# Kernel optimization log

Hardware: AMD Instinct MI355X
Metric: run time of the kernel (lower is better)

Reference implementation:

```python
import jax, jax.numpy as jnp
import numpy as np


def setup_inputs() -> dict:
    key = jax.random.key(0)
    k1, k2 = jax.random.split(key)
    B, T, C = 32, 1024, 384
    MAX_LEN = 8192
    x = jax.random.normal(k1, (B, T, C), dtype=jnp.float32)
    duration = jax.random.randint(k2, (B, T), 0, 8, dtype=jnp.int64)
    return {"x": x, "duration": duration, "max_len": MAX_LEN}


def reference(x, duration, max_len):
    # x: [B, T, C] float; duration: [B, T] int frame counts; max_len: python int.
    # Equivalent of per-row repeat_interleave(x, duration) followed by zero-pad
    # to max_len, done as one fused cumsum + searchsorted + gather.
    B, T, C = x.shape
    cum = jnp.cumsum(duration, axis=1)            # [B, T] end frame of each phoneme
    mel_len = cum[:, -1]                          # [B] total expanded length
    pos = jnp.arange(max_len)                     # [max_len] output frame indices
    # For output frame j, source phoneme = first i with cum[i] > j
    idx = jax.vmap(lambda c: jnp.searchsorted(c, pos, side="right"))(cum)  # [B, max_len]
    idx = jnp.minimum(idx, T - 1)
    mask = pos[None, :] < mel_len[:, None]        # [B, max_len] valid (non-pad) frames
    out = jnp.take_along_axis(x, idx[:, :, None], axis=1)  # [B, max_len, C]
    out = jnp.where(mask[:, :, None], out, jnp.zeros((), dtype=x.dtype))
    return out, mel_len
```

## Files before the change

### kernel.cpp

```cpp
#include <hip/hip_runtime.h>


#define BB 32
#define TT 1024
#define CC 384
#define MAXLEN 8192
#define OUT0 (BB * MAXLEN * CC)

typedef float f32x4 __attribute__((ext_vector_type(4)));

__global__ void lr_prep(const int* __restrict__ dur,
                        int* __restrict__ idx,
                        float* __restrict__ mel_out) {
    __shared__ int lds[TT];
    const int b = blockIdx.x;
    const int t = threadIdx.x;
    lds[t] = dur[b * TT + t];
    __syncthreads();
    for (int off = 1; off < TT; off <<= 1) {
        int v = (t >= off) ? lds[t - off] : 0;
        __syncthreads();
        lds[t] += v;
        __syncthreads();
    }
    const int ml = lds[TT - 1];
    if (t == TT - 1) mel_out[b] = (float)ml;

    #pragma unroll
    for (int k = 0; k < MAXLEN / TT; ++k) {
        int p = t + k * TT;
        int r = -1;
        if (p < ml) {
            int lo = 0, hi = TT;
            while (lo < hi) {
                int mid = (lo + hi) >> 1;
                if (lds[mid] <= p) lo = mid + 1; else hi = mid;
            }
            r = (lo < TT - 1) ? lo : (TT - 1);
        }
        idx[b * MAXLEN + p] = r;
    }
}

__global__ void lr_gather(const f32x4* __restrict__ x4,
                          const int* __restrict__ idx,
                          f32x4* __restrict__ out4) {
    const unsigned QPR = CC / 4;
    const unsigned HALF = (unsigned)BB * MAXLEN * QPR / 2;
    const unsigned stride = gridDim.x * blockDim.x;
    for (unsigned q = blockIdx.x * blockDim.x + threadIdx.x; q < HALF; q += stride) {
        const unsigned q2 = q + HALF;
        unsigned row1 = q / QPR,  lane1 = q  - row1 * QPR;
        unsigned row2 = q2 / QPR, lane2 = q2 - row2 * QPR;
        int i1 = idx[row1];
        int i2 = idx[row2];
        f32x4 v1 = (f32x4)0.f, v2 = (f32x4)0.f;
        if (i1 >= 0) v1 = x4[((row1 >> 13) * TT + (unsigned)i1) * QPR + lane1];
        if (i2 >= 0) v2 = x4[((row2 >> 13) * TT + (unsigned)i2) * QPR + lane2];
        __builtin_nontemporal_store(v1, &out4[q]);
        __builtin_nontemporal_store(v2, &out4[q2]);
    }
}

extern "C" void kernel_launch(void* const* d_in, const int* in_sizes, int n_in,
                              void* d_out, int out_size, void* d_ws, size_t ws_size,
                              hipStream_t stream) {
    const float* x   = (const float*)d_in[0];
    const int*   dur = (const int*)d_in[1];
    float* out = (float*)d_out;

    int* idx = (int*)d_ws;

    lr_prep<<<BB, TT, 0, stream>>>(dur, idx, out + OUT0);
    lr_gather<<<4096, 256, 0, stream>>>((const f32x4*)x, idx, (f32x4*)out);
}
```

Before: 86.11 us.

## Fuse duration scan and gather into one per-chunk kernel

Replaces the separate prep kernel and the global idx buffer with a single kernel. Each block handles one batch row's 256-frame chunk, recomputes the duration prefix sum in LDS, binary-searches its chunk's source indices into shared memory, then streams the gather. This removes a kernel launch, the serialization between the two kernels, and the idx round trip through global memory. The cost is redundant scan work in every block, and the grid shape changes from grid-stride to fixed per-chunk tiling.

```diff
diff --git a/kernel.cpp b/kernel.cpp
--- a/kernel.cpp
+++ b/kernel.cpp
@@ -6,59 +6,73 @@
 #define CC 384
 #define MAXLEN 8192
 #define OUT0 (BB * MAXLEN * CC)
+#define NT 512
+#define ROWS_PER_BLK 256
+#define NCHUNK (MAXLEN / ROWS_PER_BLK)
+#define QPR (CC / 4)
+#define QPB (ROWS_PER_BLK * QPR)
+#define ITERS (QPB / NT)
 
 typedef float f32x4 __attribute__((ext_vector_type(4)));
 
-__global__ void lr_prep(const int* __restrict__ dur,
-                        int* __restrict__ idx,
-                        float* __restrict__ mel_out) {
-    __shared__ int lds[TT];
-    const int b = blockIdx.x;
-    const int t = threadIdx.x;
-    lds[t] = dur[b * TT + t];
+__global__ __launch_bounds__(NT) void lr_fused(const int* __restrict__ dur,
+                                               const f32x4* __restrict__ x4,
+                                               f32x4* __restrict__ out4,
+                                               float* __restrict__ mel_out) {
+    __shared__ int sd[TT];
+    __shared__ int ss[NT];
+    __shared__ int sidx[ROWS_PER_BLK];
+    const int b     = blockIdx.y;
+    const int chunk = blockIdx.x;
+    const int t     = threadIdx.x;
+
+    sd[t]      = dur[b * TT + t];
+    sd[t + NT] = dur[b * TT + t + NT];
     __syncthreads();
-    for (int off = 1; off < TT; off <<= 1) {
-        int v = (t >= off) ? lds[t - off] : 0;
+    ss[t] = sd[2 * t] + sd[2 * t + 1];
+    __syncthreads();
+    #pragma unroll
+    for (int off = 1; off < NT; off <<= 1) {
+        int v = (t >= off) ? ss[t - off] : 0;
         __syncthreads();
-        lds[t] += v;
+        ss[t] += v;
         __syncthreads();
     }
-    const int ml = lds[TT - 1];
-    if (t == TT - 1) mel_out[b] = (float)ml;
+    int inc = ss[t];
+    int d1  = sd[2 * t + 1];
+    __syncthreads();
+    sd[2 * t + 1] = inc;
+    sd[2 * t]     = inc - d1;
+    __syncthreads();
+    const int ml = sd[TT - 1];
+    if (chunk == 0 && t == 0) mel_out[b] = (float)ml;
 
-    #pragma unroll
-    for (int k = 0; k < MAXLEN / TT; ++k) {
-        int p = t + k * TT;
+    if (t < ROWS_PER_BLK) {
+        int p = chunk * ROWS_PER_BLK + t;
         int r = -1;
         if (p < ml) {
             int lo = 0, hi = TT;
             while (lo < hi) {
                 int mid = (lo + hi) >> 1;
-                if (lds[mid] <= p) lo = mid + 1; else hi = mid;
+                if (sd[mid] <= p) lo = mid + 1; else hi = mid;
             }
             r = (lo < TT - 1) ? lo : (TT - 1);
         }
-        idx[b * MAXLEN + p] = r;
+        sidx[t] = r;
     }
-}
+    __syncthreads();
 
-__global__ void lr_gather(const f32x4* __restrict__ x4,
-                          const int* __restrict__ idx,
-                          f32x4* __restrict__ out4) {
-    const unsigned QPR = CC / 4;
-    const unsigned HALF = (unsigned)BB * MAXLEN * QPR / 2;
-    const unsigned stride = gridDim.x * blockDim.x;
-    for (unsigned q = blockIdx.x * blockDim.x + threadIdx.x; q < HALF; q += stride) {
-        const unsigned q2 = q + HALF;
-        unsigned row1 = q / QPR,  lane1 = q  - row1 * QPR;
-        unsigned row2 = q2 / QPR, lane2 = q2 - row2 * QPR;
-        int i1 = idx[row1];
-        int i2 = idx[row2];
-        f32x4 v1 = (f32x4)0.f, v2 = (f32x4)0.f;
-        if (i1 >= 0) v1 = x4[((row1 >> 13) * TT + (unsigned)i1) * QPR + lane1];
-        if (i2 >= 0) v2 = x4[((row2 >> 13) * TT + (unsigned)i2) * QPR + lane2];
-        __builtin_nontemporal_store(v1, &out4[q]);
-        __builtin_nontemporal_store(v2, &out4[q2]);
+    const f32x4* __restrict__ xb = x4 + (size_t)b * TT * QPR;
+    f32x4* __restrict__ ob = out4 + (size_t)(b * MAXLEN + chunk * ROWS_PER_BLK) * QPR;
+    #pragma unroll 4
+    for (int k = 0; k < ITERS; ++k) {
+        unsigned q    = (unsigned)t + (unsigned)k * NT;
+        unsigned row  = q / QPR;
+        unsigned lane = q - row * QPR;
+        int i = sidx[row];
+        f32x4 v = (f32x4)0.f;
+        if (i >= 0) v = xb[(unsigned)i * QPR + lane];
+        __builtin_nontemporal_store(v, &ob[q]);
     }
 }
 
@@ -69,8 +83,6 @@
     const int*   dur = (const int*)d_in[1];
     float* out = (float*)d_out;
 
-    int* idx = (int*)d_ws;
-
-    lr_prep<<<BB, TT, 0, stream>>>(dur, idx, out + OUT0);
-    lr_gather<<<4096, 256, 0, stream>>>((const f32x4*)x, idx, (f32x4*)out);
+    dim3 grid(NCHUNK, BB);
+    lr_fused<<<grid, NT, 0, stream>>>(dur, (const f32x4*)x, (f32x4*)out, out + OUT0);
 }
```

Measured after the change: 90.80 us. +5.4%, slower.
